# Optimization experiments

Measured on AMD Instinct MI355X. Metric: run time of the kernel, lower is better.

Reference implementation:

```python
import jax, jax.numpy as jnp
import numpy as np

N_FFT = 2048
HOP = 512
N_FREQ = N_FFT // 2 + 1  # 1025


def _dft_conv_weights():
    # periodic ('fftbins=True') Hann window, matching librosa get_window('hann', N, fftbins=True)
    n = np.arange(N_FFT)
    win = 0.5 - 0.5 * np.cos(2.0 * np.pi * n / N_FFT)
    k = np.arange(N_FREQ)
    ang = 2.0 * np.pi * np.outer(k, n) / N_FFT  # (F, n_fft)
    # W[n, k] = exp(-2*pi*i*n*k/N); real part = cos, imag part = -sin; windowed per-tap
    w_real = (np.cos(ang) * win[None, :]).astype(np.float32)
    w_imag = (-np.sin(ang) * win[None, :]).astype(np.float32)
    return w_real, w_imag


def setup_inputs() -> dict:
    key = jax.random.key(0)
    x = jax.random.normal(key, (16, 320000), dtype=jnp.float32)
    w_real, w_imag = _dft_conv_weights()
    return {
        "input": x,
        "conv_real_w": jnp.asarray(w_real),
        "conv_imag_w": jnp.asarray(w_imag),
    }


def reference(input, conv_real_w, conv_imag_w):
    # center=True: reflect-pad n_fft//2 on both sides
    pad = N_FFT // 2
    x = jnp.pad(input, ((0, 0), (pad, pad)), mode="reflect")  # (B, L + n_fft)
    L = x.shape[1]
    T = (L - N_FFT) // HOP + 1  # time_steps
    # frame extraction == Conv1d with kernel n_fft, stride hop
    idx = jnp.arange(T)[:, None] * HOP + jnp.arange(N_FFT)[None, :]  # (T, n_fft)
    frames = x[:, idx]  # (B, T, n_fft)
    real = jnp.einsum("btn,fn->bft", frames, conv_real_w)  # (B, F, T)
    imag = jnp.einsum("btn,fn->bft", frames, conv_imag_w)  # (B, F, T)
    return real, imag
```

## Files before the change

### kernel.cpp

```cpp
#include <hip/hip_runtime.h>

#define B_BATCH 16
#define XLEN    320000
#define NFFT    2048
#define HOP     512
#define PADW    1024
#define NFREQ   1025
#define T_OUT   626
#define M_ROWS  2050
#define NCOLS   (B_BATCH * T_OUT)
#define MT2     17
#define NT2     40
#define NBLK    (MT2 * NT2)
#define KT2     32

#define XPAD_LEN    322048
#define XPAD_STRIDE 330240
#define APACK_BYTES ((size_t)MT2 * 64 * 8192)
#define XPAD_BYTES  ((size_t)(B_BATCH + 1) * XPAD_STRIDE * 2)
#define WS_NEEDED   (APACK_BYTES + XPAD_BYTES)

typedef __bf16 bf16x8 __attribute__((ext_vector_type(8)));
typedef __bf16 bf16x4 __attribute__((ext_vector_type(4)));
typedef float  f32x4  __attribute__((ext_vector_type(4)));

__device__ __forceinline__ void gload_lds16(const void* g, void* l) {
    __builtin_amdgcn_global_load_lds(
        (const __attribute__((address_space(1))) unsigned int*)g,
        (__attribute__((address_space(3))) unsigned int*)l,
        16, 0, 0);
}

__global__ __launch_bounds__(256) void prep_w(
    const float* __restrict__ wre, const float* __restrict__ wim,
    __bf16* __restrict__ apack)
{
    const int gid   = blockIdx.x * 256 + threadIdx.x;
    const int scell = gid & 3;
    const int row   = (gid >> 2) & 127;
    const int ph    = (gid >> 9) & 63;
    const int mt    = gid >> 15;

    const int grow = mt * 128 + row;
    const int k    = ph * 32 + (((scell ^ (row >> 1)) & 3) << 3);

    bf16x8 v = bf16x8{};
    if (grow < M_ROWS) {
        const float* src = (grow < NFREQ)
            ? (wre + (size_t)grow * NFFT + k)
            : (wim + (size_t)(grow - NFREQ) * NFFT + k);
        const float4 a = *reinterpret_cast<const float4*>(src);
        const float4 b = *reinterpret_cast<const float4*>(src + 4);
        v[0] = (__bf16)a.x; v[1] = (__bf16)a.y; v[2] = (__bf16)a.z; v[3] = (__bf16)a.w;
        v[4] = (__bf16)b.x; v[5] = (__bf16)b.y; v[6] = (__bf16)b.z; v[7] = (__bf16)b.w;
    }
    *reinterpret_cast<bf16x8*>(apack + (size_t)gid * 8) = v;
}

__global__ __launch_bounds__(256) void prep_x(
    const float* __restrict__ x, __bf16* __restrict__ xpad)
{
    const int gid = blockIdx.x * 256 + threadIdx.x;
    if (gid >= (B_BATCH + 1) * (XPAD_STRIDE / 8)) return;
    const int b  = gid / (XPAD_STRIDE / 8);
    const int i0 = (gid - b * (XPAD_STRIDE / 8)) * 8;

    bf16x8 v = bf16x8{};
    if (b < B_BATCH) {
        const float* xb = x + (size_t)b * XLEN;
        const int pos0 = i0 - PADW;
        if (pos0 >= 0 && pos0 + 8 <= XLEN) {
            const float4 a = *reinterpret_cast<const float4*>(xb + pos0);
            const float4 c = *reinterpret_cast<const float4*>(xb + pos0 + 4);
            v[0] = (__bf16)a.x; v[1] = (__bf16)a.y; v[2] = (__bf16)a.z; v[3] = (__bf16)a.w;
            v[4] = (__bf16)c.x; v[5] = (__bf16)c.y; v[6] = (__bf16)c.z; v[7] = (__bf16)c.w;
        } else {
            #pragma unroll
            for (int e = 0; e < 8; ++e) {
                const int i = i0 + e;
                if (i >= XPAD_LEN) { v[e] = (__bf16)0.f; continue; }
                int p = i - PADW;
                p = (p < 0) ? -p : p;
                p = (p >= XLEN) ? (2 * XLEN - 2 - p) : p;
                v[e] = (__bf16)xb[p];
            }
        }
    }
    *reinterpret_cast<bf16x8*>(xpad + (size_t)b * XPAD_STRIDE + i0) = v;
}


#define MFMA16 __builtin_amdgcn_mfma_f32_16x16x32_bf16

#define VM6 asm volatile("s_waitcnt vmcnt(6)" ::: "memory");
#define VM0 asm volatile("s_waitcnt vmcnt(0)" ::: "memory");

#define STGM(PH_, SLOT_) {                                                        \
    const char* as_ = ablk + ((size_t)(PH_) << 13);                               \
    unsigned char* ad_ = lds + ((SLOT_) << 13) + (wid << 10);                     \
    gload_lds16(as_, ad_);                                                        \
    gload_lds16(as_ + 4096, ad_ + 4096);                                          \
    const int ko_ = (PH_) << 6;                                                   \
    unsigned char* bd_ = lds + 24576 + ((SLOT_) << 14) + (wid << 10);             \
    gload_lds16(gb0 + ko_, bd_);                                                  \
    gload_lds16(gb1 + ko_, bd_ + 4096);                                           \
    gload_lds16(gb2 + ko_, bd_ + 8192);                                           \
    gload_lds16(gb3 + ko_, bd_ + 12288);                                          \
}

#define DSRD(SLN_, FA_, FB_) {                                                    \
    const unsigned ab_ = ((unsigned)(SLN_) << 13) + offA_base;                    \
    const unsigned bb_ = 24576u + ((unsigned)(SLN_) << 14) + offB_base;           \
    _Pragma("unroll")                                                             \
    for (int m_ = 0; m_ < 4; ++m_)                                                \
        FA_[m_] = *(const bf16x8*)(lds + ab_ + (m_ << 10));                       \
    _Pragma("unroll")                                                             \
    for (int n_ = 0; n_ < 8; ++n_)                                                \
        FB_[n_] = *(const bf16x8*)(lds + bb_ + (n_ << 10));                       \
}

#define CLUSTER(FA_, FB_) {                                                       \
    __builtin_amdgcn_s_setprio(1);                                                \
    _Pragma("unroll")                                                             \
    for (int m_ = 0; m_ < 4; ++m_)                                                \
        _Pragma("unroll")                                                         \
        for (int n_ = 0; n_ < 8; ++n_)                                            \
            acc[m_][n_] = MFMA16(FA_[m_], FB_[n_], acc[m_][n_], 0, 0, 0);         \
    __builtin_amdgcn_s_setprio(0);                                                \
}

#define PHASE(SLN_, STG_, VMW_, CFA_, CFB_, NFA_, NFB_) {                         \
    STG_                                                                          \
    VMW_                                                                          \
    __builtin_amdgcn_s_barrier();                                                 \
    __builtin_amdgcn_sched_barrier(0);                                            \
    DSRD(SLN_, NFA_, NFB_)                                                        \
    CLUSTER(CFA_, CFB_)                                                           \
    asm volatile("s_waitcnt lgkmcnt(0)" ::: "memory");                            \
    __builtin_amdgcn_sched_barrier(0);                                            \
}

__global__ __launch_bounds__(256, 2) void stft_gemm6(
    const __bf16* __restrict__ apack,
    const __bf16* __restrict__ xpad,
    float* __restrict__ out)
{
    __shared__ __align__(16) unsigned char lds[73728];

    const int tid  = threadIdx.x;
    const int lane = tid & 63;
    const int wid  = tid >> 6;
    const int wm   = wid >> 1;
    const int wn   = wid & 1;
    const int fr   = lane & 15;
    const int kq   = lane >> 4;

    const int orig = (blockIdx.x & 7) * 85 + (blockIdx.x >> 3);
    const int nt = orig / MT2;
    const int mt = orig % MT2;

    const char* ablk = (const char*)apack + (size_t)mt * (64 * 8192) + (size_t)tid * 16;

    const char* xpb = (const char*)xpad;
    const char* gb0; const char* gb1; const char* gb2; const char* gb3;
    {
        const int r0 = tid >> 2;
        const int sc = (tid & 3) ^ ((r0 >> 1) & 3);
        #pragma unroll
        for (int j = 0; j < 4; ++j) {
            const int col = nt * 256 + r0 + 64 * j;
            const unsigned b = (unsigned)col / 626u;
            const int tc = col - (int)b * 626;
            const char* p = xpb + ((size_t)b * XPAD_STRIDE + (size_t)tc * 512) * 2 + sc * 16;
            if (j == 0) gb0 = p; else if (j == 1) gb1 = p;
            else if (j == 2) gb2 = p; else gb3 = p;
        }
    }

    const unsigned swz = (unsigned)(((kq ^ (fr >> 1)) & 3) << 4);
    const unsigned offA_base = (unsigned)((wm * 64 + fr) * 64) + swz;
    const unsigned offB_base = (unsigned)((wn * 128 + fr) * 64) + swz;

    f32x4 acc[4][8];
    #pragma unroll
    for (int m = 0; m < 4; ++m)
        #pragma unroll
        for (int n = 0; n < 8; ++n)
            acc[m][n] = f32x4{0.f, 0.f, 0.f, 0.f};

    bf16x8 faP[4], fbP[8], faQ[4], fbQ[8];

    STGM(0, 0)
    STGM(1, 1)
    VM6
    __builtin_amdgcn_s_barrier();
    __builtin_amdgcn_sched_barrier(0);
    DSRD(0, faP, fbP)
    asm volatile("s_waitcnt lgkmcnt(0)" ::: "memory");
    __builtin_amdgcn_sched_barrier(0);

    #pragma unroll 1
    for (int i = 0; i < 10; ++i) {
        const int t = 6 * i;
        PHASE(1, STGM(t + 2, 2), VM6, faP, fbP, faQ, fbQ)
        PHASE(2, STGM(t + 3, 0), VM6, faQ, fbQ, faP, fbP)
        PHASE(0, STGM(t + 4, 1), VM6, faP, fbP, faQ, fbQ)
        PHASE(1, STGM(t + 5, 2), VM6, faQ, fbQ, faP, fbP)
        PHASE(2, STGM(t + 6, 0), VM6, faP, fbP, faQ, fbQ)
        PHASE(0, STGM(t + 7, 1), VM6, faQ, fbQ, faP, fbP)
    }
    PHASE(1, STGM(62, 2), VM6, faP, fbP, faQ, fbQ)
    PHASE(2, STGM(63, 0), VM6, faQ, fbQ, faP, fbP)
    PHASE(0, , VM0,            faP, fbP, faQ, fbQ)
    CLUSTER(faQ, fbQ)

    const size_t imag_base = (size_t)B_BATCH * NFREQ * T_OUT;
    #pragma unroll
    for (int n = 0; n < 8; ++n) {
        const int col = nt * 256 + wn * 128 + n * 16 + fr;
        if (col < NCOLS) {
            const unsigned b = (unsigned)col / 626u;
            const int tc = col - (int)b * 626;
            const size_t colbase = (size_t)b * NFREQ * T_OUT + (size_t)tc;
            #pragma unroll
            for (int m = 0; m < 4; ++m) {
                #pragma unroll
                for (int j = 0; j < 4; ++j) {
                    const int grow = mt * 128 + wm * 64 + m * 16 + kq * 4 + j;
                    if (grow < M_ROWS) {
                        const size_t off = (grow < NFREQ)
                            ? colbase + (size_t)grow * T_OUT
                            : imag_base + colbase + (size_t)(grow - NFREQ) * T_OUT;
                        out[off] = acc[m][n][j];
                    }
                }
            }
        }
    }
}

__device__ __forceinline__ unsigned lds_off_fb(int row, int kbyte) {
    return (unsigned)(row * 128 + (kbyte ^ ((row & 7) << 4)));
}

__global__ __launch_bounds__(256) void stft_gemm_fb(
    const float* __restrict__ x,
    const float* __restrict__ wre,
    const float* __restrict__ wim,
    float* __restrict__ out)
{
    __shared__ __align__(16) unsigned char ldsA[128 * 128];
    __shared__ __align__(16) unsigned char ldsB[128 * 128];

    const int tid  = threadIdx.x;
    const int lane = tid & 63;
    const int wid  = tid >> 6;
    const int wmf  = wid >> 1;
    const int wnf  = wid & 1;

    const int bid = blockIdx.x;
    const int b   = bid / (17 * 5);
    const int rem = bid % (17 * 5);
    const int mt  = rem / 5;
    const int nt  = rem % 5;

    const int row0 = mt * 128;
    const int col0 = nt * 128;
    const float* xb = x + (size_t)b * XLEN;

    const int c4 = (tid & 15) * 4;
    const int r0 = tid >> 4;

    f32x4 acc[4][4];
    #pragma unroll
    for (int m = 0; m < 4; ++m)
        #pragma unroll
        for (int n = 0; n < 4; ++n)
            acc[m][n] = f32x4{0.f, 0.f, 0.f, 0.f};

    const int fr = lane & 15;
    const int kq = lane >> 4;

    for (int k0 = 0; k0 < NFFT; k0 += 64) {
        bf16x4 sa[8], sb[8];
        #pragma unroll
        for (int rr = 0; rr < 8; ++rr) {
            const int row  = rr * 16 + r0;
            const int grow = row0 + row;
            float4 v = make_float4(0.f, 0.f, 0.f, 0.f);
            if (grow < M_ROWS) {
                const float* wsrc = (grow < NFREQ)
                    ? (wre + (size_t)grow * NFFT)
                    : (wim + (size_t)(grow - NFREQ) * NFFT);
                v = *reinterpret_cast<const float4*>(wsrc + k0 + c4);
            }
            sa[rr].x = (__bf16)v.x; sa[rr].y = (__bf16)v.y;
            sa[rr].z = (__bf16)v.z; sa[rr].w = (__bf16)v.w;
        }
        #pragma unroll
        for (int rr = 0; rr < 8; ++rr) {
            const int trow = rr * 16 + r0;
            const int t    = col0 + trow;
            float4 v = make_float4(0.f, 0.f, 0.f, 0.f);
            if (t < T_OUT) {
                const int pos = t * HOP + k0 + c4 - PADW;
                if (pos >= 0 && pos <= XLEN - 4) {
                    v = *reinterpret_cast<const float4*>(xb + pos);
                } else {
                    float tmp[4];
                    #pragma unroll
                    for (int e = 0; e < 4; ++e) {
                        int p = pos + e;
                        p = (p < 0) ? -p : p;
                        p = (p >= XLEN) ? (2 * XLEN - 2 - p) : p;
                        tmp[e] = xb[p];
                    }
                    v = make_float4(tmp[0], tmp[1], tmp[2], tmp[3]);
                }
            }
            sb[rr].x = (__bf16)v.x; sb[rr].y = (__bf16)v.y;
            sb[rr].z = (__bf16)v.z; sb[rr].w = (__bf16)v.w;
        }
        __syncthreads();
        #pragma unroll
        for (int rr = 0; rr < 8; ++rr) {
            const int row = rr * 16 + r0;
            *reinterpret_cast<bf16x4*>(ldsA + lds_off_fb(row, c4 * 2)) = sa[rr];
            *reinterpret_cast<bf16x4*>(ldsB + lds_off_fb(row, c4 * 2)) = sb[rr];
        }
        __syncthreads();
        #pragma unroll
        for (int kk = 0; kk < 2; ++kk) {
            const int kbyte = kk * 64 + kq * 16;
            bf16x8 af[4], bfv[4];
            #pragma unroll
            for (int m = 0; m < 4; ++m)
                af[m] = *reinterpret_cast<const bf16x8*>(
                    ldsA + lds_off_fb(wmf * 64 + m * 16 + fr, kbyte));
            #pragma unroll
            for (int n = 0; n < 4; ++n)
                bfv[n] = *reinterpret_cast<const bf16x8*>(
                    ldsB + lds_off_fb(wnf * 64 + n * 16 + fr, kbyte));
            #pragma unroll
            for (int m = 0; m < 4; ++m)
                #pragma unroll
                for (int n = 0; n < 4; ++n)
                    acc[m][n] = MFMA16(af[m], bfv[n], acc[m][n], 0, 0, 0);
        }
    }

    const size_t imag_base = (size_t)B_BATCH * NFREQ * T_OUT;
    #pragma unroll
    for (int m = 0; m < 4; ++m) {
        #pragma unroll
        for (int n = 0; n < 4; ++n) {
            #pragma unroll
            for (int j = 0; j < 4; ++j) {
                const int grow = row0 + wmf * 64 + m * 16 + kq * 4 + j;
                const int gcol = col0 + wnf * 64 + n * 16 + fr;
                if (grow < M_ROWS && gcol < T_OUT) {
                    size_t off;
                    if (grow < NFREQ)
                        off = ((size_t)b * NFREQ + grow) * T_OUT + gcol;
                    else
                        off = imag_base + ((size_t)b * NFREQ + (grow - NFREQ)) * T_OUT + gcol;
                    out[off] = acc[m][n][j];
                }
            }
        }
    }
}

extern "C" void kernel_launch(void* const* d_in, const int* in_sizes, int n_in,
                              void* d_out, int out_size, void* d_ws, size_t ws_size,
                              hipStream_t stream) {
    const float* x   = (const float*)d_in[0];
    const float* wre = (const float*)d_in[1];
    const float* wim = (const float*)d_in[2];
    float* out = (float*)d_out;

    if (ws_size < WS_NEEDED) {
        stft_gemm_fb<<<dim3(B_BATCH * 17 * 5), 256, 0, stream>>>(x, wre, wim, out);
        return;
    }

    __bf16* apack = (__bf16*)d_ws;
    __bf16* xpad  = (__bf16*)((char*)d_ws + APACK_BYTES);

    prep_w<<<dim3(557056 / 256), 256, 0, stream>>>(wre, wim, apack);
    prep_x<<<dim3(((B_BATCH + 1) * (XPAD_STRIDE / 8) + 255) / 256), 256, 0, stream>>>(x, xpad);
    stft_gemm6<<<dim3(NBLK), 256, 0, stream>>>(apack, xpad, out);
}
```

Measured before the change: 136.0 us.

## Use 8-wave blocks with smaller per-wave tiles and drop register double-buffering

The GEMM kernel goes from 4 waves per 256-thread block to 8 waves per 512-thread block. Each wave now computes a 64x64 output sub-tile instead of 64x128, so the 128x256 block tile is split across more waves and each thread issues fewer global-to-LDS loads per stage. The P/Q register double-buffering of fragments is removed: each phase reads its LDS fragments, issues the next stage's prefetch, waits, and then runs 16 MFMAs. This trades register-level prefetch for more waves per CU to hide latency, which means more barriers per unit of work and less MFMA work between syncs.

```diff
diff --git a/kernel.cpp b/kernel.cpp
--- a/kernel.cpp
+++ b/kernel.cpp
@@ -92,55 +92,60 @@
 
 #define MFMA16 __builtin_amdgcn_mfma_f32_16x16x32_bf16
 
-#define VM6 asm volatile("s_waitcnt vmcnt(6)" ::: "memory");
+#define VM3 asm volatile("s_waitcnt vmcnt(3)" ::: "memory");
 #define VM0 asm volatile("s_waitcnt vmcnt(0)" ::: "memory");
 
-#define STGM(PH_, SLOT_) {                                                        \
-    const char* as_ = ablk + ((size_t)(PH_) << 13);                               \
-    unsigned char* ad_ = lds + ((SLOT_) << 13) + (wid << 10);                     \
-    gload_lds16(as_, ad_);                                                        \
-    gload_lds16(as_ + 4096, ad_ + 4096);                                          \
-    const int ko_ = (PH_) << 6;                                                   \
-    unsigned char* bd_ = lds + 24576 + ((SLOT_) << 14) + (wid << 10);             \
-    gload_lds16(gb0 + ko_, bd_);                                                  \
-    gload_lds16(gb1 + ko_, bd_ + 4096);                                           \
-    gload_lds16(gb2 + ko_, bd_ + 8192);                                           \
-    gload_lds16(gb3 + ko_, bd_ + 12288);                                          \
-}
-
-#define DSRD(SLN_, FA_, FB_) {                                                    \
-    const unsigned ab_ = ((unsigned)(SLN_) << 13) + offA_base;                    \
-    const unsigned bb_ = 24576u + ((unsigned)(SLN_) << 14) + offB_base;           \
-    _Pragma("unroll")                                                             \
-    for (int m_ = 0; m_ < 4; ++m_)                                                \
-        FA_[m_] = *(const bf16x8*)(lds + ab_ + (m_ << 10));                       \
-    _Pragma("unroll")                                                             \
-    for (int n_ = 0; n_ < 8; ++n_)                                                \
-        FB_[n_] = *(const bf16x8*)(lds + bb_ + (n_ << 10));                       \
-}
-
-#define CLUSTER(FA_, FB_) {                                                       \
-    __builtin_amdgcn_s_setprio(1);                                                \
-    _Pragma("unroll")                                                             \
-    for (int m_ = 0; m_ < 4; ++m_)                                                \
-        _Pragma("unroll")                                                         \
-        for (int n_ = 0; n_ < 8; ++n_)                                            \
-            acc[m_][n_] = MFMA16(FA_[m_], FB_[n_], acc[m_][n_], 0, 0, 0);         \
-    __builtin_amdgcn_s_setprio(0);                                                \
-}
-
-#define PHASE(SLN_, STG_, VMW_, CFA_, CFB_, NFA_, NFB_) {                         \
+#define STG(PH_, SLOT_) {                                                         \
+    gload_lds16(ablk + ((size_t)(PH_) << 13),                                     \
+                lds + ((SLOT_) << 13) + (wid << 10));                             \
+    {                                                                             \
+        const int ko_ = (PH_) << 6;                                               \
+        unsigned char* d_ = lds + 24576 + ((SLOT_) << 14) + (wid << 10);          \
+        gload_lds16(gb0 + ko_, d_);                                               \
+        gload_lds16(gb1 + ko_, d_ + 8192);                                        \
+    }                                                                             \
+}
+
+#define PH(SLOT_, STG_, VMW_) {                                                   \
+    bf16x8 a0, a1, a2, a3, b0, b1, b2, b3;                                        \
+    {                                                                             \
+        const unsigned ab_ = ((unsigned)(SLOT_) << 13) + offA_base;               \
+        const unsigned bb_ = 24576u + ((unsigned)(SLOT_) << 14) + offB_base;      \
+        a0 = *(const bf16x8*)(lds + ab_);                                         \
+        a1 = *(const bf16x8*)(lds + ab_ + 1024);                                  \
+        a2 = *(const bf16x8*)(lds + ab_ + 2048);                                  \
+        a3 = *(const bf16x8*)(lds + ab_ + 3072);                                  \
+        b0 = *(const bf16x8*)(lds + bb_);                                         \
+        b1 = *(const bf16x8*)(lds + bb_ + 1024);                                  \
+        b2 = *(const bf16x8*)(lds + bb_ + 2048);                                  \
+        b3 = *(const bf16x8*)(lds + bb_ + 3072);                                  \
+    }                                                                             \
     STG_                                                                          \
     VMW_                                                                          \
     __builtin_amdgcn_s_barrier();                                                 \
-    __builtin_amdgcn_sched_barrier(0);                                            \
-    DSRD(SLN_, NFA_, NFB_)                                                        \
-    CLUSTER(CFA_, CFB_)                                                           \
     asm volatile("s_waitcnt lgkmcnt(0)" ::: "memory");                            \
     __builtin_amdgcn_sched_barrier(0);                                            \
-}
-
-__global__ __launch_bounds__(256, 2) void stft_gemm6(
+    __builtin_amdgcn_s_setprio(1);                                                \
+    acc[0][0] = MFMA16(a0, b0, acc[0][0], 0, 0, 0);                               \
+    acc[0][1] = MFMA16(a0, b1, acc[0][1], 0, 0, 0);                               \
+    acc[0][2] = MFMA16(a0, b2, acc[0][2], 0, 0, 0);                               \
+    acc[0][3] = MFMA16(a0, b3, acc[0][3], 0, 0, 0);                               \
+    acc[1][0] = MFMA16(a1, b0, acc[1][0], 0, 0, 0);                               \
+    acc[1][1] = MFMA16(a1, b1, acc[1][1], 0, 0, 0);                               \
+    acc[1][2] = MFMA16(a1, b2, acc[1][2], 0, 0, 0);                               \
+    acc[1][3] = MFMA16(a1, b3, acc[1][3], 0, 0, 0);                               \
+    acc[2][0] = MFMA16(a2, b0, acc[2][0], 0, 0, 0);                               \
+    acc[2][1] = MFMA16(a2, b1, acc[2][1], 0, 0, 0);                               \
+    acc[2][2] = MFMA16(a2, b2, acc[2][2], 0, 0, 0);                               \
+    acc[2][3] = MFMA16(a2, b3, acc[2][3], 0, 0, 0);                               \
+    acc[3][0] = MFMA16(a3, b0, acc[3][0], 0, 0, 0);                               \
+    acc[3][1] = MFMA16(a3, b1, acc[3][1], 0, 0, 0);                               \
+    acc[3][2] = MFMA16(a3, b2, acc[3][2], 0, 0, 0);                               \
+    acc[3][3] = MFMA16(a3, b3, acc[3][3], 0, 0, 0);                               \
+    __builtin_amdgcn_s_setprio(0);                                                \
+}
+
+__global__ __launch_bounds__(512, 4) void stft_gemm7(
     const __bf16* __restrict__ apack,
     const __bf16* __restrict__ xpad,
     float* __restrict__ out)
@@ -150,8 +155,8 @@
     const int tid  = threadIdx.x;
     const int lane = tid & 63;
     const int wid  = tid >> 6;
-    const int wm   = wid >> 1;
-    const int wn   = wid & 1;
+    const int wm   = wid >> 2;
+    const int wn   = wid & 3;
     const int fr   = lane & 15;
     const int kq   = lane >> 4;
 
@@ -162,62 +167,57 @@
     const char* ablk = (const char*)apack + (size_t)mt * (64 * 8192) + (size_t)tid * 16;
 
     const char* xpb = (const char*)xpad;
-    const char* gb0; const char* gb1; const char* gb2; const char* gb3;
+    const char* gb0;
+    const char* gb1;
     {
         const int r0 = tid >> 2;
         const int sc = (tid & 3) ^ ((r0 >> 1) & 3);
-        #pragma unroll
-        for (int j = 0; j < 4; ++j) {
-            const int col = nt * 256 + r0 + 64 * j;
-            const unsigned b = (unsigned)col / 626u;
-            const int tc = col - (int)b * 626;
-            const char* p = xpb + ((size_t)b * XPAD_STRIDE + (size_t)tc * 512) * 2 + sc * 16;
-            if (j == 0) gb0 = p; else if (j == 1) gb1 = p;
-            else if (j == 2) gb2 = p; else gb3 = p;
-        }
+        int col = nt * 256 + r0;
+        unsigned b = (unsigned)col / 626u;
+        int tc = col - (int)b * 626;
+        gb0 = xpb + ((size_t)b * XPAD_STRIDE + (size_t)tc * 512) * 2 + sc * 16;
+        col += 128;
+        b = (unsigned)col / 626u;
+        tc = col - (int)b * 626;
+        gb1 = xpb + ((size_t)b * XPAD_STRIDE + (size_t)tc * 512) * 2 + sc * 16;
     }
 
     const unsigned swz = (unsigned)(((kq ^ (fr >> 1)) & 3) << 4);
     const unsigned offA_base = (unsigned)((wm * 64 + fr) * 64) + swz;
-    const unsigned offB_base = (unsigned)((wn * 128 + fr) * 64) + swz;
-
-    f32x4 acc[4][8];
+    const unsigned offB_base = (unsigned)((wn * 64 + fr) * 64) + swz;
+
+    f32x4 acc[4][4];
     #pragma unroll
     for (int m = 0; m < 4; ++m)
         #pragma unroll
-        for (int n = 0; n < 8; ++n)
+        for (int n = 0; n < 4; ++n)
             acc[m][n] = f32x4{0.f, 0.f, 0.f, 0.f};
 
-    bf16x8 faP[4], fbP[8], faQ[4], fbQ[8];
-
-    STGM(0, 0)
-    STGM(1, 1)
-    VM6
+    STG(0, 0)
+    STG(1, 1)
+    VM3
     __builtin_amdgcn_s_barrier();
-    __builtin_amdgcn_sched_barrier(0);
-    DSRD(0, faP, fbP)
-    asm volatile("s_waitcnt lgkmcnt(0)" ::: "memory");
     __builtin_amdgcn_sched_barrier(0);
 
     #pragma unroll 1
     for (int i = 0; i < 10; ++i) {
         const int t = 6 * i;
-        PHASE(1, STGM(t + 2, 2), VM6, faP, fbP, faQ, fbQ)
-        PHASE(2, STGM(t + 3, 0), VM6, faQ, fbQ, faP, fbP)
-        PHASE(0, STGM(t + 4, 1), VM6, faP, fbP, faQ, fbQ)
-        PHASE(1, STGM(t + 5, 2), VM6, faQ, fbQ, faP, fbP)
-        PHASE(2, STGM(t + 6, 0), VM6, faP, fbP, faQ, fbQ)
-        PHASE(0, STGM(t + 7, 1), VM6, faQ, fbQ, faP, fbP)
-    }
-    PHASE(1, STGM(62, 2), VM6, faP, fbP, faQ, fbQ)
-    PHASE(2, STGM(63, 0), VM6, faQ, fbQ, faP, fbP)
-    PHASE(0, , VM0,            faP, fbP, faQ, fbQ)
-    CLUSTER(faQ, fbQ)
+        PH(0, STG(t + 2, 2), VM3)
+        PH(1, STG(t + 3, 0), VM3)
+        PH(2, STG(t + 4, 1), VM3)
+        PH(0, STG(t + 5, 2), VM3)
+        PH(1, STG(t + 6, 0), VM3)
+        PH(2, STG(t + 7, 1), VM3)
+    }
+    PH(0, STG(62, 2), VM3)
+    PH(1, STG(63, 0), VM3)
+    PH(2, , VM0)
+    PH(0, , )
 
     const size_t imag_base = (size_t)B_BATCH * NFREQ * T_OUT;
     #pragma unroll
-    for (int n = 0; n < 8; ++n) {
-        const int col = nt * 256 + wn * 128 + n * 16 + fr;
+    for (int n = 0; n < 4; ++n) {
+        const int col = nt * 256 + wn * 64 + n * 16 + fr;
         if (col < NCOLS) {
             const unsigned b = (unsigned)col / 626u;
             const int tc = col - (int)b * 626;
@@ -389,5 +389,5 @@
 
     prep_w<<<dim3(557056 / 256), 256, 0, stream>>>(wre, wim, apack);
     prep_x<<<dim3(((B_BATCH + 1) * (XPAD_STRIDE / 8) + 255) / 256), 256, 0, stream>>>(x, xpad);
-    stft_gemm6<<<dim3(NBLK), 256, 0, stream>>>(apack, xpad, out);
-}
+    stft_gemm7<<<dim3(NBLK), 512, 0, stream>>>(apack, xpad, out);
+}
```

Measured after the change: 113.7 us. 1.2x faster.

## Retile STFT GEMM to 256x128 blocks with 512 threads and 64-deep k-steps

Applied to the files above, without the earlier changes.

Replaces the 128x256, 256-thread GEMM with a 256x128 tile computed by 8 waves, using 64-wide k tiles double-buffered in LDS and split into two MFMA half-phases per step. The weight packing kernel is rewritten for the new 256-row tile layout with an 8-way XOR swizzle, and the block-to-XCD mapping is recomputed for 711 blocks. The intent is to raise per-block reuse and occupancy. In exchange it adds barriers and full vmcnt(0) waits each step, which reduces load-latency hiding compared to the old three-slot ring, and the larger LDS footprint may limit blocks per CU.

```diff
diff --git a/kernel.cpp b/kernel.cpp
--- a/kernel.cpp
+++ b/kernel.cpp
@@ -9,14 +9,14 @@
 #define T_OUT   626
 #define M_ROWS  2050
 #define NCOLS   (B_BATCH * T_OUT)
-#define MT2     17
-#define NT2     40
-#define NBLK    (MT2 * NT2)
+#define MT3     9
+#define NT3     79
+#define NBLK3   (MT3 * NT3)
 #define KT2     32
 
 #define XPAD_LEN    322048
 #define XPAD_STRIDE 330240
-#define APACK_BYTES ((size_t)MT2 * 64 * 8192)
+#define APACK_BYTES ((size_t)MT3 * 32 * 2 * 16384)
 #define XPAD_BYTES  ((size_t)(B_BATCH + 1) * XPAD_STRIDE * 2)
 #define WS_NEEDED   (APACK_BYTES + XPAD_BYTES)
 
@@ -35,14 +35,15 @@
     const float* __restrict__ wre, const float* __restrict__ wim,
     __bf16* __restrict__ apack)
 {
-    const int gid   = blockIdx.x * 256 + threadIdx.x;
-    const int scell = gid & 3;
-    const int row   = (gid >> 2) & 127;
-    const int ph    = (gid >> 9) & 63;
-    const int mt    = gid >> 15;
-
-    const int grow = mt * 128 + row;
-    const int k    = ph * 32 + (((scell ^ (row >> 1)) & 3) << 3);
+    const int gid  = blockIdx.x * 256 + threadIdx.x;
+    const int cell = gid & 7;
+    const int row  = (gid >> 3) & 127;
+    const int half = (gid >> 10) & 1;
+    const int kt   = (gid >> 11) & 31;
+    const int mt   = gid >> 16;
+
+    const int grow = mt * 256 + half * 128 + row;
+    const int k    = kt * 64 + ((cell ^ (row & 7)) << 3);
 
     bf16x8 v = bf16x8{};
     if (grow < M_ROWS) {
@@ -91,61 +92,94 @@
 
 
 #define MFMA16 __builtin_amdgcn_mfma_f32_16x16x32_bf16
-
-#define VM6 asm volatile("s_waitcnt vmcnt(6)" ::: "memory");
 #define VM0 asm volatile("s_waitcnt vmcnt(0)" ::: "memory");
 
-#define STGM(PH_, SLOT_) {                                                        \
-    const char* as_ = ablk + ((size_t)(PH_) << 13);                               \
-    unsigned char* ad_ = lds + ((SLOT_) << 13) + (wid << 10);                     \
-    gload_lds16(as_, ad_);                                                        \
-    gload_lds16(as_ + 4096, ad_ + 4096);                                          \
-    const int ko_ = (PH_) << 6;                                                   \
-    unsigned char* bd_ = lds + 24576 + ((SLOT_) << 14) + (wid << 10);             \
-    gload_lds16(gb0 + ko_, bd_);                                                  \
-    gload_lds16(gb1 + ko_, bd_ + 4096);                                           \
-    gload_lds16(gb2 + ko_, bd_ + 8192);                                           \
-    gload_lds16(gb3 + ko_, bd_ + 12288);                                          \
-}
-
-#define DSRD(SLN_, FA_, FB_) {                                                    \
-    const unsigned ab_ = ((unsigned)(SLN_) << 13) + offA_base;                    \
-    const unsigned bb_ = 24576u + ((unsigned)(SLN_) << 14) + offB_base;           \
-    _Pragma("unroll")                                                             \
-    for (int m_ = 0; m_ < 4; ++m_)                                                \
-        FA_[m_] = *(const bf16x8*)(lds + ab_ + (m_ << 10));                       \
-    _Pragma("unroll")                                                             \
-    for (int n_ = 0; n_ < 8; ++n_)                                                \
-        FB_[n_] = *(const bf16x8*)(lds + bb_ + (n_ << 10));                       \
-}
-
-#define CLUSTER(FA_, FB_) {                                                       \
+#define STGT(KT_, BUF_) {                                                         \
+    const char* as_ = ablk + (size_t)(KT_) * 32768;                               \
+    unsigned char* ad_ = lds + (BUF_) + (wid << 10);                              \
+    gload_lds16(as_,         ad_);                                                \
+    gload_lds16(as_ + 8192,  ad_ + 8192);                                         \
+    gload_lds16(as_ + 16384, ad_ + 16384);                                        \
+    gload_lds16(as_ + 24576, ad_ + 24576);                                        \
+    const int ko_ = (KT_) << 7;                                                   \
+    gload_lds16(gb0 + ko_, lds + (BUF_) + 32768 + (wid << 10));                   \
+    gload_lds16(gb1 + ko_, lds + (BUF_) + 40960 + (wid << 10));                   \
+}
+
+#define PHA(BUF_, STG_) {                                                         \
+    a00 = *(const bf16x8*)(lds + (BUF_) + aoff0);                                 \
+    a01 = *(const bf16x8*)(lds + (BUF_) + aoff1);                                 \
+    a10 = *(const bf16x8*)(lds + (BUF_) + aoff0 + 2048);                          \
+    a11 = *(const bf16x8*)(lds + (BUF_) + aoff1 + 2048);                          \
+    a20 = *(const bf16x8*)(lds + (BUF_) + aoff0 + 4096);                          \
+    a21 = *(const bf16x8*)(lds + (BUF_) + aoff1 + 4096);                          \
+    a30 = *(const bf16x8*)(lds + (BUF_) + aoff0 + 6144);                          \
+    a31 = *(const bf16x8*)(lds + (BUF_) + aoff1 + 6144);                          \
+    bf16x8 b00 = *(const bf16x8*)(lds + (BUF_) + boff0);                          \
+    bf16x8 b01 = *(const bf16x8*)(lds + (BUF_) + boff1);                          \
+    bf16x8 b10 = *(const bf16x8*)(lds + (BUF_) + boff0 + 2048);                   \
+    bf16x8 b11 = *(const bf16x8*)(lds + (BUF_) + boff1 + 2048);                   \
+    STG_                                                                          \
+    __builtin_amdgcn_s_barrier();                                                 \
+    asm volatile("s_waitcnt lgkmcnt(0)" ::: "memory");                            \
+    __builtin_amdgcn_sched_barrier(0);                                            \
     __builtin_amdgcn_s_setprio(1);                                                \
-    _Pragma("unroll")                                                             \
-    for (int m_ = 0; m_ < 4; ++m_)                                                \
-        _Pragma("unroll")                                                         \
-        for (int n_ = 0; n_ < 8; ++n_)                                            \
-            acc[m_][n_] = MFMA16(FA_[m_], FB_[n_], acc[m_][n_], 0, 0, 0);         \
+    acc[0][0] = MFMA16(a00, b00, acc[0][0], 0, 0, 0);                             \
+    acc[0][0] = MFMA16(a01, b01, acc[0][0], 0, 0, 0);                             \
+    acc[1][0] = MFMA16(a10, b00, acc[1][0], 0, 0, 0);                             \
+    acc[1][0] = MFMA16(a11, b01, acc[1][0], 0, 0, 0);                             \
+    acc[2][0] = MFMA16(a20, b00, acc[2][0], 0, 0, 0);                             \
+    acc[2][0] = MFMA16(a21, b01, acc[2][0], 0, 0, 0);                             \
+    acc[3][0] = MFMA16(a30, b00, acc[3][0], 0, 0, 0);                             \
+    acc[3][0] = MFMA16(a31, b01, acc[3][0], 0, 0, 0);                             \
+    acc[0][1] = MFMA16(a00, b10, acc[0][1], 0, 0, 0);                             \
+    acc[0][1] = MFMA16(a01, b11, acc[0][1], 0, 0, 0);                             \
+    acc[1][1] = MFMA16(a10, b10, acc[1][1], 0, 0, 0);                             \
+    acc[1][1] = MFMA16(a11, b11, acc[1][1], 0, 0, 0);                             \
+    acc[2][1] = MFMA16(a20, b10, acc[2][1], 0, 0, 0);                             \
+    acc[2][1] = MFMA16(a21, b11, acc[2][1], 0, 0, 0);                             \
+    acc[3][1] = MFMA16(a30, b10, acc[3][1], 0, 0, 0);                             \
+    acc[3][1] = MFMA16(a31, b11, acc[3][1], 0, 0, 0);                             \
     __builtin_amdgcn_s_setprio(0);                                                \
-}
-
-#define PHASE(SLN_, STG_, VMW_, CFA_, CFB_, NFA_, NFB_) {                         \
-    STG_                                                                          \
+    __builtin_amdgcn_s_barrier();                                                 \
+}
+
+#define PHB(BUF_, VMW_) {                                                         \
+    bf16x8 b20 = *(const bf16x8*)(lds + (BUF_) + boff0 + 4096);                   \
+    bf16x8 b21 = *(const bf16x8*)(lds + (BUF_) + boff1 + 4096);                   \
+    bf16x8 b30 = *(const bf16x8*)(lds + (BUF_) + boff0 + 6144);                   \
+    bf16x8 b31 = *(const bf16x8*)(lds + (BUF_) + boff1 + 6144);                   \
     VMW_                                                                          \
     __builtin_amdgcn_s_barrier();                                                 \
-    __builtin_amdgcn_sched_barrier(0);                                            \
-    DSRD(SLN_, NFA_, NFB_)                                                        \
-    CLUSTER(CFA_, CFB_)                                                           \
     asm volatile("s_waitcnt lgkmcnt(0)" ::: "memory");                            \
     __builtin_amdgcn_sched_barrier(0);                                            \
-}
-
-__global__ __launch_bounds__(256, 2) void stft_gemm6(
+    __builtin_amdgcn_s_setprio(1);                                                \
+    acc[0][2] = MFMA16(a00, b20, acc[0][2], 0, 0, 0);                             \
+    acc[0][2] = MFMA16(a01, b21, acc[0][2], 0, 0, 0);                             \
+    acc[1][2] = MFMA16(a10, b20, acc[1][2], 0, 0, 0);                             \
+    acc[1][2] = MFMA16(a11, b21, acc[1][2], 0, 0, 0);                             \
+    acc[2][2] = MFMA16(a20, b20, acc[2][2], 0, 0, 0);                             \
+    acc[2][2] = MFMA16(a21, b21, acc[2][2], 0, 0, 0);                             \
+    acc[3][2] = MFMA16(a30, b20, acc[3][2], 0, 0, 0);                             \
+    acc[3][2] = MFMA16(a31, b21, acc[3][2], 0, 0, 0);                             \
+    acc[0][3] = MFMA16(a00, b30, acc[0][3], 0, 0, 0);                             \
+    acc[0][3] = MFMA16(a01, b31, acc[0][3], 0, 0, 0);                             \
+    acc[1][3] = MFMA16(a10, b30, acc[1][3], 0, 0, 0);                             \
+    acc[1][3] = MFMA16(a11, b31, acc[1][3], 0, 0, 0);                             \
+    acc[2][3] = MFMA16(a20, b30, acc[2][3], 0, 0, 0);                             \
+    acc[2][3] = MFMA16(a21, b31, acc[2][3], 0, 0, 0);                             \
+    acc[3][3] = MFMA16(a30, b30, acc[3][3], 0, 0, 0);                             \
+    acc[3][3] = MFMA16(a31, b31, acc[3][3], 0, 0, 0);                             \
+    __builtin_amdgcn_s_setprio(0);                                                \
+    __builtin_amdgcn_s_barrier();                                                 \
+}
+
+__global__ __launch_bounds__(512, 2) void stft_gemm11(
     const __bf16* __restrict__ apack,
     const __bf16* __restrict__ xpad,
     float* __restrict__ out)
 {
-    __shared__ __align__(16) unsigned char lds[73728];
+    __shared__ __align__(16) unsigned char lds[98304];
 
     const int tid  = threadIdx.x;
     const int lane = tid & 63;
@@ -155,69 +189,73 @@
     const int fr   = lane & 15;
     const int kq   = lane >> 4;
 
-    const int orig = (blockIdx.x & 7) * 85 + (blockIdx.x >> 3);
-    const int nt = orig / MT2;
-    const int mt = orig % MT2;
-
-    const char* ablk = (const char*)apack + (size_t)mt * (64 * 8192) + (size_t)tid * 16;
+    int G;
+    {
+        const int L = blockIdx.x;
+        const int xcd = L & 7;
+        const int pos = L >> 3;
+        G = (xcd < 7) ? xcd * 89 + pos : 623 + pos;
+    }
+    const int mt = G / NT3;
+    const int nt = G - mt * NT3;
+
+    const char* ablk = (const char*)apack + (size_t)mt * 1048576 + (size_t)tid * 16;
 
     const char* xpb = (const char*)xpad;
-    const char* gb0; const char* gb1; const char* gb2; const char* gb3;
+    const char* gb0;
+    const char* gb1;
     {
-        const int r0 = tid >> 2;
-        const int sc = (tid & 3) ^ ((r0 >> 1) & 3);
-        #pragma unroll
-        for (int j = 0; j < 4; ++j) {
-            const int col = nt * 256 + r0 + 64 * j;
+        const int cellb = tid & 7;
+        #pragma unroll
+        for (int j = 0; j < 2; ++j) {
+            const int brow = j * 64 + (tid >> 3);
+            const int col  = nt * 128 + brow;
             const unsigned b = (unsigned)col / 626u;
             const int tc = col - (int)b * 626;
-            const char* p = xpb + ((size_t)b * XPAD_STRIDE + (size_t)tc * 512) * 2 + sc * 16;
-            if (j == 0) gb0 = p; else if (j == 1) gb1 = p;
-            else if (j == 2) gb2 = p; else gb3 = p;
-        }
-    }
-
-    const unsigned swz = (unsigned)(((kq ^ (fr >> 1)) & 3) << 4);
-    const unsigned offA_base = (unsigned)((wm * 64 + fr) * 64) + swz;
-    const unsigned offB_base = (unsigned)((wn * 128 + fr) * 64) + swz;
-
-    f32x4 acc[4][8];
+            const char* p = xpb + (size_t)b * (XPAD_STRIDE * 2) + (size_t)tc * 1024
+                            + ((cellb ^ (brow & 7)) << 4);
+            if (j == 0) gb0 = p; else gb1 = p;
+        }
+    }
+
+    const int f7 = fr & 7;
+    const unsigned aoff0 = (unsigned)((wm >> 1) * 16384 + ((wm & 1) * 64 + fr) * 128
+                                      + ((kq ^ f7) << 4));
+    const unsigned aoff1 = (unsigned)((wm >> 1) * 16384 + ((wm & 1) * 64 + fr) * 128
+                                      + (((4 + kq) ^ f7) << 4));
+    const unsigned boff0 = (unsigned)(32768 + (wn * 64 + fr) * 128 + ((kq ^ f7) << 4));
+    const unsigned boff1 = (unsigned)(32768 + (wn * 64 + fr) * 128 + (((4 + kq) ^ f7) << 4));
+
+    f32x4 acc[4][4];
     #pragma unroll
     for (int m = 0; m < 4; ++m)
         #pragma unroll
-        for (int n = 0; n < 8; ++n)
+        for (int n = 0; n < 4; ++n)
             acc[m][n] = f32x4{0.f, 0.f, 0.f, 0.f};
 
-    bf16x8 faP[4], fbP[8], faQ[4], fbQ[8];
-
-    STGM(0, 0)
-    STGM(1, 1)
-    VM6
+    bf16x8 a00, a01, a10, a11, a20, a21, a30, a31;
+
+    STGT(0, 0)
+    VM0
     __builtin_amdgcn_s_barrier();
     __builtin_amdgcn_sched_barrier(0);
-    DSRD(0, faP, fbP)
-    asm volatile("s_waitcnt lgkmcnt(0)" ::: "memory");
-    __builtin_amdgcn_sched_barrier(0);
 
     #pragma unroll 1
-    for (int i = 0; i < 10; ++i) {
-        const int t = 6 * i;
-        PHASE(1, STGM(t + 2, 2), VM6, faP, fbP, faQ, fbQ)
-        PHASE(2, STGM(t + 3, 0), VM6, faQ, fbQ, faP, fbP)
-        PHASE(0, STGM(t + 4, 1), VM6, faP, fbP, faQ, fbQ)
-        PHASE(1, STGM(t + 5, 2), VM6, faQ, fbQ, faP, fbP)
-        PHASE(2, STGM(t + 6, 0), VM6, faP, fbP, faQ, fbQ)
-        PHASE(0, STGM(t + 7, 1), VM6, faQ, fbQ, faP, fbP)
-    }
-    PHASE(1, STGM(62, 2), VM6, faP, fbP, faQ, fbQ)
-    PHASE(2, STGM(63, 0), VM6, faQ, fbQ, faP, fbP)
-    PHASE(0, , VM0,            faP, fbP, faQ, fbQ)
-    CLUSTER(faQ, fbQ)
+    for (int i = 0; i < 15; ++i) {
+        PHA(0,     STGT(2 * i + 1, 49152))
+        PHB(0,     VM0)
+        PHA(49152, STGT(2 * i + 2, 0))
+        PHB(49152, VM0)
+    }
+    PHA(0,     STGT(31, 49152))
+    PHB(0,     VM0)
+    PHA(49152, )
+    PHB(49152, )
 
     const size_t imag_base = (size_t)B_BATCH * NFREQ * T_OUT;
     #pragma unroll
-    for (int n = 0; n < 8; ++n) {
-        const int col = nt * 256 + wn * 128 + n * 16 + fr;
+    for (int n = 0; n < 4; ++n) {
+        const int col = nt * 128 + wn * 64 + n * 16 + fr;
         if (col < NCOLS) {
             const unsigned b = (unsigned)col / 626u;
             const int tc = col - (int)b * 626;
@@ -226,7 +264,7 @@
             for (int m = 0; m < 4; ++m) {
                 #pragma unroll
                 for (int j = 0; j < 4; ++j) {
-                    const int grow = mt * 128 + wm * 64 + m * 16 + kq * 4 + j;
+                    const int grow = mt * 256 + wm * 64 + m * 16 + kq * 4 + j;
                     if (grow < M_ROWS) {
                         const size_t off = (grow < NFREQ)
                             ? colbase + (size_t)grow * T_OUT
@@ -387,7 +425,7 @@
     __bf16* apack = (__bf16*)d_ws;
     __bf16* xpad  = (__bf16*)((char*)d_ws + APACK_BYTES);
 
-    prep_w<<<dim3(557056 / 256), 256, 0, stream>>>(wre, wim, apack);
+    prep_w<<<dim3(589824 / 256), 256, 0, stream>>>(wre, wim, apack);
     prep_x<<<dim3(((B_BATCH + 1) * (XPAD_STRIDE / 8) + 255) / 256), 256, 0, stream>>>(x, xpad);
-    stft_gemm6<<<dim3(NBLK), 256, 0, stream>>>(apack, xpad, out);
-}
+    stft_gemm11<<<dim3(NBLK3), 512, 0, stream>>>(apack, xpad, out);
+}
```

Measured after the change: 142.9 us. 5.1% more time.
